# Optimization experiments

Measured on AMD Instinct MI355X. Metric: run time of the kernel, lower is better.

Reference implementation:

```python
import jax, jax.numpy as jnp
import numpy as np

E, B, S, H = 8, 16, 512, 1024
LN_EPS = 1e-12


def setup_inputs() -> dict:
    key = jax.random.key(0)
    k = jax.random.split(key, 5)
    return {
        "hidden_states": jax.random.normal(k[0], (B, S, H), dtype=jnp.float32),
        "input_tensor": jax.random.normal(k[1], (B, S, H), dtype=jnp.float32),
        "expert_idx": jax.random.randint(k[2], (B,), 0, E, dtype=jnp.int64)
        if jax.config.jax_enable_x64 else jax.random.randint(k[2], (B,), 0, E, dtype=jnp.int32),
        "W": jax.random.normal(k[3], (E, H, H), dtype=jnp.float32) * (1.0 / np.sqrt(H)),
        "b": jax.random.normal(k[4], (E, H), dtype=jnp.float32) * 0.02,
        "gamma": jnp.ones((H,), dtype=jnp.float32),
        "beta": jnp.zeros((H,), dtype=jnp.float32),
    }


def reference(hidden_states, input_tensor, expert_idx, W, b, gamma, beta):
    # All-expert dense forward, matching single_select_fwd's stacked compute.
    # all_out: [E, B, S, H]
    all_out = jnp.einsum("bsh,ehd->ebsd", hidden_states, W) + b[:, None, None, :]
    # slice_for_expert: pick (expert_idx[b], b) for each batch row -> [B, S, H]
    selected = all_out[expert_idx, jnp.arange(hidden_states.shape[0])]
    # dropout is identity in eval mode; residual + LayerNorm
    x = selected + input_tensor
    mu = jnp.mean(x, axis=-1, keepdims=True)
    var = jnp.mean(jnp.square(x - mu), axis=-1, keepdims=True)
    return (x - mu) * jax.lax.rsqrt(var + LN_EPS) * gamma + beta
```

## Files before the change

kernel.cpp:

```cpp
#include <hip/hip_runtime.h>
#include <hip/hip_bf16.h>

#define BB 16
#define SS 512
#define HH 1024

typedef __attribute__((ext_vector_type(8))) short bhalf8;
typedef __attribute__((ext_vector_type(16))) float f32x16;

static __device__ __forceinline__ unsigned int pack2(float a, float b) {
    __hip_bfloat162 h = __float22bfloat162_rn(make_float2(a, b));
    union { __hip_bfloat162 h; unsigned int u; } cv;
    cv.h = h;
    return cv.u;
}

__global__ __launch_bounds__(256, 2)
void moe_gemm_kernel(const float* __restrict__ hid, const float* __restrict__ inp,
                     const int* __restrict__ eidx, const float* __restrict__ W,
                     const float* __restrict__ bias, float* __restrict__ out)
{
    __shared__ unsigned short As[128 * 40];
    __shared__ unsigned short Ws[128 * 40];

    int bx  = blockIdx.x;
    int swz = (bx & 7) * 64 + (bx >> 3);
    int bt   = swz >> 5;
    int tile = swz & 31;
    int mt = tile >> 3;
    int nt = tile & 7;

    int e = eidx[bt];

    int t    = threadIdx.x;
    int wave = t >> 6;
    int lane = t & 63;
    int l31  = lane & 31;
    int g    = lane >> 5;
    int wm = wave >> 1, wn = wave & 1;

    const float* aptr[4];
    int a_lds[4];
#pragma unroll
    for (int i = 0; i < 4; ++i) {
        int f = t + i * 256;
        int row = f >> 3, c4 = f & 7;
        aptr[i]  = hid + (size_t)(bt * SS + mt * 128 + row) * HH + c4 * 4;
        a_lds[i] = row * 40 + c4 * 4;
    }
    int kb = t & 7, db = t >> 3;
    const float* wptr = W + (size_t)e * HH * HH + (size_t)(kb * 4) * HH + nt * 128 + db * 4;

    float4 areg[4];
    float4 wreg[4];

#pragma unroll
    for (int i = 0; i < 4; ++i)
        areg[i] = *reinterpret_cast<const float4*>(aptr[i]);
#pragma unroll
    for (int r = 0; r < 4; ++r)
        wreg[r] = *reinterpret_cast<const float4*>(wptr + (size_t)r * HH);

    f32x16 acc[4] = {};

    for (int ks = 0; ks < 32; ++ks) {
        __syncthreads();
#pragma unroll
        for (int i = 0; i < 4; ++i) {
            unsigned int u0 = pack2(areg[i].x, areg[i].y);
            unsigned int u1 = pack2(areg[i].z, areg[i].w);
            *reinterpret_cast<uint2*>(&As[a_lds[i]]) = make_uint2(u0, u1);
        }
#pragma unroll
        for (int c = 0; c < 4; ++c) {
            float c0 = (&wreg[0].x)[c];
            float c1 = (&wreg[1].x)[c];
            float c2 = (&wreg[2].x)[c];
            float c3 = (&wreg[3].x)[c];
            unsigned int u0 = pack2(c0, c1);
            unsigned int u1 = pack2(c2, c3);
            *reinterpret_cast<uint2*>(&Ws[(db * 4 + c) * 40 + kb * 4]) = make_uint2(u0, u1);
        }
        __syncthreads();

        if (ks < 31) {
            int k0 = (ks + 1) * 32;
#pragma unroll
            for (int i = 0; i < 4; ++i)
                areg[i] = *reinterpret_cast<const float4*>(aptr[i] + k0);
#pragma unroll
            for (int r = 0; r < 4; ++r)
                wreg[r] = *reinterpret_cast<const float4*>(wptr + (size_t)(k0 + r) * HH);
        }

#pragma unroll
        for (int kh = 0; kh < 2; ++kh) {
            bhalf8 af[2], bf[2];
#pragma unroll
            for (int mf = 0; mf < 2; ++mf)
                af[mf] = *reinterpret_cast<const bhalf8*>(
                    &As[(wm * 64 + mf * 32 + l31) * 40 + kh * 16 + g * 8]);
#pragma unroll
            for (int nf = 0; nf < 2; ++nf)
                bf[nf] = *reinterpret_cast<const bhalf8*>(
                    &Ws[(wn * 64 + nf * 32 + l31) * 40 + kh * 16 + g * 8]);
#pragma unroll
            for (int mf = 0; mf < 2; ++mf)
#pragma unroll
                for (int nf = 0; nf < 2; ++nf)
                    acc[mf * 2 + nf] = __builtin_amdgcn_mfma_f32_32x32x16_bf16(
                        af[mf], bf[nf], acc[mf * 2 + nf], 0, 0, 0);
        }
    }

    int srow0 = bt * SS + mt * 128 + wm * 64;
    int dcol0 = nt * 128 + wn * 64;
#pragma unroll
    for (int mf = 0; mf < 2; ++mf)
#pragma unroll
        for (int nf = 0; nf < 2; ++nf) {
            f32x16 a = acc[mf * 2 + nf];
            int dcol = dcol0 + nf * 32 + l31;
            float bv = bias[e * HH + dcol];
#pragma unroll
            for (int r = 0; r < 16; ++r) {
                int srow = srow0 + mf * 32 + (r & 3) + 8 * (r >> 2) + 4 * g;
                size_t off = (size_t)srow * HH + dcol;
                out[off] = a[r] + bv + inp[off];
            }
        }
}

__global__ __launch_bounds__(256)
void ln_kernel(float* __restrict__ x, const float* __restrict__ gamma,
               const float* __restrict__ beta)
{
    int row = blockIdx.x;
    int t = threadIdx.x;
    size_t base = (size_t)row * HH + t * 4;
    float4 v = *reinterpret_cast<const float4*>(&x[base]);
    float s1 = v.x + v.y + v.z + v.w;
    float s2 = v.x * v.x + v.y * v.y + v.z * v.z + v.w * v.w;
#pragma unroll
    for (int off = 32; off > 0; off >>= 1) {
        s1 += __shfl_xor(s1, off, 64);
        s2 += __shfl_xor(s2, off, 64);
    }
    __shared__ float red[8];
    if ((t & 63) == 0) { red[(t >> 6) * 2] = s1; red[(t >> 6) * 2 + 1] = s2; }
    __syncthreads();
    float S1 = red[0] + red[2] + red[4] + red[6];
    float S2 = red[1] + red[3] + red[5] + red[7];
    float mean = S1 * (1.0f / HH);
    float var  = S2 * (1.0f / HH) - mean * mean;
    float rs = rsqrtf(var + 1e-12f);
    float4 gv = *reinterpret_cast<const float4*>(&gamma[t * 4]);
    float4 bv = *reinterpret_cast<const float4*>(&beta[t * 4]);
    float4 o;
    o.x = (v.x - mean) * rs * gv.x + bv.x;
    o.y = (v.y - mean) * rs * gv.y + bv.y;
    o.z = (v.z - mean) * rs * gv.z + bv.z;
    o.w = (v.w - mean) * rs * gv.w + bv.w;
    *reinterpret_cast<float4*>(&x[base]) = o;
}

extern "C" void kernel_launch(void* const* d_in, const int* in_sizes, int n_in,
                              void* d_out, int out_size, void* d_ws, size_t ws_size,
                              hipStream_t stream) {
    const float* hid   = (const float*)d_in[0];
    const float* inp   = (const float*)d_in[1];
    const int*   eidx  = (const int*)d_in[2];
    const float* W     = (const float*)d_in[3];
    const float* bias  = (const float*)d_in[4];
    const float* gamma = (const float*)d_in[5];
    const float* beta  = (const float*)d_in[6];
    float* out = (float*)d_out;

    moe_gemm_kernel<<<512, 256, 0, stream>>>(hid, inp, eidx, W, bias, out);
    ln_kernel<<<BB * SS, 256, 0, stream>>>(out, gamma, beta);
}
```

Before: 65.29 us.

## Pre-convert used expert weights to bf16, async LDS loads, fuse LN stats into GEMM

Adds a prep kernel that converts and transposes the weights of only the selected experts to bf16 in workspace and zeroes a row-statistics buffer. The GEMM now stages tiles with global_load_lds into double-buffered, XOR-swizzled shared memory and switches to 16x16x32 MFMAs. Its epilogue computes per-row sum and sum-of-squares and accumulates them with atomics, so the LayerNorm pass only normalizes. In exchange it adds a third launch, a full weight conversion pass each call, fp32-to-bf16 packing of A in the inner loop, and atomic contention on the row sums.

```diff
diff --git a/kernel.cpp b/kernel.cpp
--- a/kernel.cpp
+++ b/kernel.cpp
@@ -5,8 +5,8 @@
 #define SS 512
 #define HH 1024
 
+typedef __attribute__((ext_vector_type(4))) float f32x4;
 typedef __attribute__((ext_vector_type(8))) short bhalf8;
-typedef __attribute__((ext_vector_type(16))) float f32x16;
 
 static __device__ __forceinline__ unsigned int pack2(float a, float b) {
     __hip_bfloat162 h = __float22bfloat162_rn(make_float2(a, b));
@@ -15,152 +15,190 @@
     return cv.u;
 }
 
+__global__ __launch_bounds__(256)
+void prep_kernel(const float* __restrict__ W, const int* __restrict__ eidx,
+                 unsigned short* __restrict__ Wt, float* __restrict__ sums)
+{
+    int bid = blockIdx.x;
+    int t = threadIdx.x;
+    if (bid < 2048) {
+        int e  = bid >> 8;
+        bool used = false;
+        for (int b = 0; b < BB; ++b) used = used || (eidx[b] == e);
+        if (!used) return;
+        int rem = bid & 255;
+        int kt = rem >> 3, dt = rem & 7;
+        int kb = t & 7, db = t >> 3;
+        const float* src = W + ((size_t)e << 20) + (size_t)(kt * 32 + kb * 4) * HH + dt * 128 + db * 4;
+        float4 r0 = *(const float4*)(src);
+        float4 r1 = *(const float4*)(src + HH);
+        float4 r2 = *(const float4*)(src + 2 * HH);
+        float4 r3 = *(const float4*)(src + 3 * HH);
+        unsigned short* dst = Wt + ((size_t)e << 20) + (size_t)(dt * 128 + db * 4) * HH + kt * 32 + kb * 4;
+#pragma unroll
+        for (int c = 0; c < 4; ++c) {
+            float c0 = (&r0.x)[c], c1 = (&r1.x)[c], c2 = (&r2.x)[c], c3 = (&r3.x)[c];
+            *reinterpret_cast<uint2*>(dst + (size_t)c * HH) =
+                make_uint2(pack2(c0, c1), pack2(c2, c3));
+        }
+    } else {
+        int i = (bid - 2048) * 1024 + t * 4;
+        float4 z = {0.f, 0.f, 0.f, 0.f};
+        *reinterpret_cast<float4*>(&sums[i]) = z;
+    }
+}
+
 __global__ __launch_bounds__(256, 2)
 void moe_gemm_kernel(const float* __restrict__ hid, const float* __restrict__ inp,
-                     const int* __restrict__ eidx, const float* __restrict__ W,
-                     const float* __restrict__ bias, float* __restrict__ out)
+                     const int* __restrict__ eidx, const unsigned short* __restrict__ Wt,
+                     const float* __restrict__ bias, float* __restrict__ sums,
+                     float* __restrict__ out)
 {
-    __shared__ unsigned short As[128 * 40];
-    __shared__ unsigned short Ws[128 * 40];
+    __shared__ char lds[49152];
 
     int bx  = blockIdx.x;
     int swz = (bx & 7) * 64 + (bx >> 3);
     int bt   = swz >> 5;
     int tile = swz & 31;
-    int mt = tile >> 3;
-    int nt = tile & 7;
-
+    int mt = tile >> 3, nt = tile & 7;
     int e = eidx[bt];
 
-    int t    = threadIdx.x;
-    int wave = t >> 6;
-    int lane = t & 63;
-    int l31  = lane & 31;
-    int g    = lane >> 5;
+    int t = threadIdx.x, wave = t >> 6, lane = t & 63;
+    int l15 = lane & 15, g = lane >> 4;
     int wm = wave >> 1, wn = wave & 1;
 
-    const float* aptr[4];
-    int a_lds[4];
+    const float* asrc[4];
+    int aoff[4];
 #pragma unroll
     for (int i = 0; i < 4; ++i) {
-        int f = t + i * 256;
-        int row = f >> 3, c4 = f & 7;
-        aptr[i]  = hid + (size_t)(bt * SS + mt * 128 + row) * HH + c4 * 4;
-        a_lds[i] = row * 40 + c4 * 4;
-    }
-    int kb = t & 7, db = t >> 3;
-    const float* wptr = W + (size_t)e * HH * HH + (size_t)(kb * 4) * HH + nt * 128 + db * 4;
-
-    float4 areg[4];
-    float4 wreg[4];
-
-#pragma unroll
-    for (int i = 0; i < 4; ++i)
-        areg[i] = *reinterpret_cast<const float4*>(aptr[i]);
-#pragma unroll
-    for (int r = 0; r < 4; ++r)
-        wreg[r] = *reinterpret_cast<const float4*>(wptr + (size_t)r * HH);
-
-    f32x16 acc[4] = {};
+        int c = t + i * 256;
+        int row = c >> 3, sp = c & 7, s = sp ^ (row & 7);
+        asrc[i] = hid + (size_t)(bt * SS + mt * 128 + row) * HH + s * 4;
+        aoff[i] = c * 16;
+    }
+    const unsigned short* wsrc[2];
+    int woff[2];
+#pragma unroll
+    for (int i = 0; i < 2; ++i) {
+        int c = t + i * 256;
+        int row = c >> 2, sp = c & 3;
+        wsrc[i] = Wt + ((size_t)e << 20) + (size_t)(nt * 128 + row) * HH + sp * 8;
+        woff[i] = c * 16;
+    }
+
+    auto stage = [&](int ks, int sel) {
+#pragma unroll
+        for (int i = 0; i < 4; ++i)
+            __builtin_amdgcn_global_load_lds(
+                (const __attribute__((address_space(1))) void*)(asrc[i] + ks * 32),
+                (__attribute__((address_space(3))) void*)(lds + sel * 16384 + aoff[i]),
+                16, 0, 0);
+#pragma unroll
+        for (int i = 0; i < 2; ++i)
+            __builtin_amdgcn_global_load_lds(
+                (const __attribute__((address_space(1))) void*)(wsrc[i] + ks * 32),
+                (__attribute__((address_space(3))) void*)(lds + 32768 + sel * 8192 + woff[i]),
+                16, 0, 0);
+    };
+
+    f32x4 acc[4][4] = {};
+
+    stage(0, 0);
+    __syncthreads();
 
     for (int ks = 0; ks < 32; ++ks) {
+        int sel = ks & 1;
+        if (ks < 31) stage(ks + 1, sel ^ 1);
+
+        const char* Af = lds + sel * 16384;
+        const char* Wf = lds + 32768 + sel * 8192;
+
+        bhalf8 af[4], bf[4];
+#pragma unroll
+        for (int mf = 0; mf < 4; ++mf) {
+            int row  = wm * 64 + mf * 16 + l15;
+            int base = row * 128 + g * 32;
+            int sw   = (row & 7) << 4;
+            float4 f0 = *(const float4*)(Af + (base ^ sw));
+            float4 f1 = *(const float4*)(Af + ((base + 16) ^ sw));
+            union { unsigned int u[4]; bhalf8 h; } cv;
+            cv.u[0] = pack2(f0.x, f0.y); cv.u[1] = pack2(f0.z, f0.w);
+            cv.u[2] = pack2(f1.x, f1.y); cv.u[3] = pack2(f1.z, f1.w);
+            af[mf] = cv.h;
+        }
+#pragma unroll
+        for (int nf = 0; nf < 4; ++nf) {
+            int row = wn * 64 + nf * 16 + l15;
+            bf[nf] = *(const bhalf8*)(Wf + row * 64 + g * 16);
+        }
+#pragma unroll
+        for (int mf = 0; mf < 4; ++mf)
+#pragma unroll
+            for (int nf = 0; nf < 4; ++nf)
+                acc[mf][nf] = __builtin_amdgcn_mfma_f32_16x16x32_bf16(
+                    af[mf], bf[nf], acc[mf][nf], 0, 0, 0);
         __syncthreads();
-#pragma unroll
-        for (int i = 0; i < 4; ++i) {
-            unsigned int u0 = pack2(areg[i].x, areg[i].y);
-            unsigned int u1 = pack2(areg[i].z, areg[i].w);
-            *reinterpret_cast<uint2*>(&As[a_lds[i]]) = make_uint2(u0, u1);
-        }
-#pragma unroll
-        for (int c = 0; c < 4; ++c) {
-            float c0 = (&wreg[0].x)[c];
-            float c1 = (&wreg[1].x)[c];
-            float c2 = (&wreg[2].x)[c];
-            float c3 = (&wreg[3].x)[c];
-            unsigned int u0 = pack2(c0, c1);
-            unsigned int u1 = pack2(c2, c3);
-            *reinterpret_cast<uint2*>(&Ws[(db * 4 + c) * 40 + kb * 4]) = make_uint2(u0, u1);
-        }
-        __syncthreads();
-
-        if (ks < 31) {
-            int k0 = (ks + 1) * 32;
-#pragma unroll
-            for (int i = 0; i < 4; ++i)
-                areg[i] = *reinterpret_cast<const float4*>(aptr[i] + k0);
-#pragma unroll
-            for (int r = 0; r < 4; ++r)
-                wreg[r] = *reinterpret_cast<const float4*>(wptr + (size_t)(k0 + r) * HH);
-        }
-
-#pragma unroll
-        for (int kh = 0; kh < 2; ++kh) {
-            bhalf8 af[2], bf[2];
-#pragma unroll
-            for (int mf = 0; mf < 2; ++mf)
-                af[mf] = *reinterpret_cast<const bhalf8*>(
-                    &As[(wm * 64 + mf * 32 + l31) * 40 + kh * 16 + g * 8]);
-#pragma unroll
-            for (int nf = 0; nf < 2; ++nf)
-                bf[nf] = *reinterpret_cast<const bhalf8*>(
-                    &Ws[(wn * 64 + nf * 32 + l31) * 40 + kh * 16 + g * 8]);
-#pragma unroll
-            for (int mf = 0; mf < 2; ++mf)
-#pragma unroll
-                for (int nf = 0; nf < 2; ++nf)
-                    acc[mf * 2 + nf] = __builtin_amdgcn_mfma_f32_32x32x16_bf16(
-                        af[mf], bf[nf], acc[mf * 2 + nf], 0, 0, 0);
-        }
-    }
-
-    int srow0 = bt * SS + mt * 128 + wm * 64;
-    int dcol0 = nt * 128 + wn * 64;
-#pragma unroll
-    for (int mf = 0; mf < 2; ++mf)
-#pragma unroll
-        for (int nf = 0; nf < 2; ++nf) {
-            f32x16 a = acc[mf * 2 + nf];
-            int dcol = dcol0 + nf * 32 + l31;
-            float bv = bias[e * HH + dcol];
-#pragma unroll
-            for (int r = 0; r < 16; ++r) {
-                int srow = srow0 + mf * 32 + (r & 3) + 8 * (r >> 2) + 4 * g;
+    }
+
+    int brow = bt * SS + mt * 128;
+#pragma unroll
+    for (int nf = 0; nf < 4; ++nf) {
+        int dcol = nt * 128 + wn * 64 + nf * 16 + l15;
+        float bv = bias[e * HH + dcol];
+#pragma unroll
+        for (int mf = 0; mf < 4; ++mf)
+#pragma unroll
+            for (int j = 0; j < 4; ++j) {
+                int srow = brow + wm * 64 + mf * 16 + g * 4 + j;
                 size_t off = (size_t)srow * HH + dcol;
-                out[off] = a[r] + bv + inp[off];
+                float v = acc[mf][nf][j] + bv + inp[off];
+                acc[mf][nf][j] = v;
+                out[off] = v;
+            }
+    }
+
+#pragma unroll
+    for (int mf = 0; mf < 4; ++mf)
+#pragma unroll
+        for (int j = 0; j < 4; ++j) {
+            float s1 = 0.f, s2 = 0.f;
+#pragma unroll
+            for (int nf = 0; nf < 4; ++nf) {
+                float v = acc[mf][nf][j];
+                s1 += v; s2 += v * v;
+            }
+#pragma unroll
+            for (int m = 8; m >= 1; m >>= 1) {
+                s1 += __shfl_xor(s1, m, 64);
+                s2 += __shfl_xor(s2, m, 64);
+            }
+            if (l15 == 0) {
+                int r = brow + wm * 64 + mf * 16 + g * 4 + j;
+                atomicAdd(&sums[r * 2], s1);
+                atomicAdd(&sums[r * 2 + 1], s2);
             }
         }
 }
 
 __global__ __launch_bounds__(256)
-void ln_kernel(float* __restrict__ x, const float* __restrict__ gamma,
-               const float* __restrict__ beta)
+void ln_apply(float* __restrict__ x, const float* __restrict__ sums,
+              const float* __restrict__ gamma, const float* __restrict__ beta)
 {
     int row = blockIdx.x;
     int t = threadIdx.x;
+    float s1 = sums[row * 2], s2 = sums[row * 2 + 1];
+    float mu  = s1 * (1.0f / HH);
+    float var = s2 * (1.0f / HH) - mu * mu;
+    float rs = rsqrtf(var + 1e-12f);
     size_t base = (size_t)row * HH + t * 4;
-    float4 v = *reinterpret_cast<const float4*>(&x[base]);
-    float s1 = v.x + v.y + v.z + v.w;
-    float s2 = v.x * v.x + v.y * v.y + v.z * v.z + v.w * v.w;
-#pragma unroll
-    for (int off = 32; off > 0; off >>= 1) {
-        s1 += __shfl_xor(s1, off, 64);
-        s2 += __shfl_xor(s2, off, 64);
-    }
-    __shared__ float red[8];
-    if ((t & 63) == 0) { red[(t >> 6) * 2] = s1; red[(t >> 6) * 2 + 1] = s2; }
-    __syncthreads();
-    float S1 = red[0] + red[2] + red[4] + red[6];
-    float S2 = red[1] + red[3] + red[5] + red[7];
-    float mean = S1 * (1.0f / HH);
-    float var  = S2 * (1.0f / HH) - mean * mean;
-    float rs = rsqrtf(var + 1e-12f);
+    float4 v  = *reinterpret_cast<const float4*>(&x[base]);
     float4 gv = *reinterpret_cast<const float4*>(&gamma[t * 4]);
     float4 bv = *reinterpret_cast<const float4*>(&beta[t * 4]);
     float4 o;
-    o.x = (v.x - mean) * rs * gv.x + bv.x;
-    o.y = (v.y - mean) * rs * gv.y + bv.y;
-    o.z = (v.z - mean) * rs * gv.z + bv.z;
-    o.w = (v.w - mean) * rs * gv.w + bv.w;
+    o.x = (v.x - mu) * rs * gv.x + bv.x;
+    o.y = (v.y - mu) * rs * gv.y + bv.y;
+    o.z = (v.z - mu) * rs * gv.z + bv.z;
+    o.w = (v.w - mu) * rs * gv.w + bv.w;
     *reinterpret_cast<float4*>(&x[base]) = o;
 }
 
@@ -176,6 +214,10 @@
     const float* beta  = (const float*)d_in[6];
     float* out = (float*)d_out;
 
-    moe_gemm_kernel<<<512, 256, 0, stream>>>(hid, inp, eidx, W, bias, out);
-    ln_kernel<<<BB * SS, 256, 0, stream>>>(out, gamma, beta);
-}
+    unsigned short* Wt = (unsigned short*)d_ws;
+    float* sums = (float*)((char*)d_ws + (16u << 20));
+
+    prep_kernel<<<2064, 256, 0, stream>>>(W, eidx, Wt, sums);
+    moe_gemm_kernel<<<512, 256, 0, stream>>>(hid, inp, eidx, Wt, bias, sums, out);
+    ln_apply<<<BB * SS, 256, 0, stream>>>(out, sums, gamma, beta);
+}
```

Result: slower. 74.41 us (+14.0%).
